# Optimization experiments

Hardware: AMD Instinct MI355X
Metric: run time of the kernel (lower is better)

Reference implementation:

```python
import jax, jax.numpy as jnp
import numpy as np

B, N, D, H, DH, DFF = 2, 2048, 1024, 16, 64, 4096
EPS = 1e-5  # F.layer_norm default


def setup_inputs() -> dict:
    key = jax.random.key(0)
    ks = jax.random.split(key, 8)
    w = lambda k, shape: jax.random.normal(k, shape, dtype=jnp.float32) * 0.02
    # standard rotary frequencies over full head dim (rot_dim = DH)
    inv_freq = 1.0 / (10000.0 ** (jnp.arange(0, DH, 2, dtype=jnp.float32) / DH))
    t = jnp.arange(N, dtype=jnp.float32)
    f = t[:, None] * inv_freq[None, :]          # [N, DH/2]
    freqs = jnp.concatenate([f, f], axis=-1)    # [N, DH]
    return {
        "x": jax.random.normal(ks[0], (B, N, D), dtype=jnp.float32),
        "gamma_pre": jnp.ones((D,), jnp.float32),
        "w_qkv": w(ks[1], (3 * D, D)),
        "w_o": w(ks[2], (D, D)),
        "gamma_ff": jnp.ones((D,), jnp.float32),
        "w_up": w(ks[3], (DFF, D)),
        "b_up": jnp.zeros((DFF,), jnp.float32),
        "w_gate": w(ks[4], (DFF, D)),
        "b_gate": jnp.zeros((DFF,), jnp.float32),
        "w_out": w(ks[5], (D, DFF)),
        "b_out": jnp.zeros((D,), jnp.float32),
        "freqs": freqs,
        "mask": jnp.ones((B, N), dtype=bool),
    }


def _layernorm(x, gamma):
    mu = jnp.mean(x, axis=-1, keepdims=True)
    var = jnp.var(x, axis=-1, keepdims=True)
    return (x - mu) * jax.lax.rsqrt(var + EPS) * gamma


def _rotate_half(x):
    x1, x2 = jnp.split(x, 2, axis=-1)
    return jnp.concatenate([-x2, x1], axis=-1)


def _rope(t, freqs):
    # rot_dim == DH so nothing is left unrotated
    return t * jnp.cos(freqs) + _rotate_half(t) * jnp.sin(freqs)


def reference(x, gamma_pre, w_qkv, w_o, gamma_ff, w_up, b_up, w_gate, b_gate,
              w_out, b_out, freqs, mask):
    b, n, d = x.shape
    # ---- self-attention branch (pre-norm) ----
    h = _layernorm(x, gamma_pre)
    qkv = h @ w_qkv.T                                   # [b, n, 3d]
    q, k, v = jnp.split(qkv, 3, axis=-1)
    to_heads = lambda t: t.reshape(b, n, H, DH).transpose(0, 2, 1, 3)  # b h n d
    q, k, v = to_heads(q), to_heads(k), to_heads(v)
    q = _rope(q, freqs)
    k = _rope(k, freqs)
    scale = 1.0 / np.sqrt(DH).astype(np.float32)
    dots = jnp.einsum('bhid,bhjd->bhij', q, k) * scale  # [b, H, n, n]
    neg = -jnp.finfo(dots.dtype).max
    dots = jnp.where(mask[:, None, None, :], dots, neg)        # key padding mask
    causal = jnp.triu(jnp.ones((n, n), dtype=bool), 1)
    dots = jnp.where(causal, neg, dots)
    attn = jax.nn.softmax(dots.astype(jnp.float32), axis=-1).astype(dots.dtype)
    o = jnp.einsum('bhij,bhjd->bhid', attn, v)
    o = o.transpose(0, 2, 1, 3).reshape(b, n, d) @ w_o.T
    o = jnp.where(mask[..., None], o, 0.0)
    x = x + o
    # ---- GLU feed-forward branch (pre-norm) ----
    h2 = _layernorm(x, gamma_ff)
    up = h2 @ w_up.T + b_up
    gate = h2 @ w_gate.T + b_gate
    ff = (up * jax.nn.silu(gate)) @ w_out.T + b_out
    return x + ff
```

## Files before the change

### kernel.cpp

```cpp
#include <hip/hip_runtime.h>
#include <stdint.h>


#define B_ 2
#define N_ 2048
#define D_ 1024
#define H_ 16
#define DFF_ 4096
#define ROWS_ (B_*N_)

typedef unsigned short u16;
typedef short short4_ __attribute__((ext_vector_type(4)));
typedef short short8 __attribute__((ext_vector_type(8)));
typedef float float4_ __attribute__((ext_vector_type(4)));

#define NEGBIG (-1e30f)
#define QSCALE 0.1803368801111204f

__device__ __forceinline__ float b2f(u16 u) {
  union { unsigned u; float f; } c; c.u = ((unsigned)u) << 16; return c.f;
}
__device__ __forceinline__ u16 f2b(float f) {
  union { float f; unsigned u; } c; c.f = f;
  unsigned x = c.u;
  x += 0x7fffu + ((x >> 16) & 1u);
  return (u16)(x >> 16);
}

__device__ __forceinline__ void gl_lds16(const u16* g, u16* l) {
  __builtin_amdgcn_global_load_lds(
      (const __attribute__((address_space(1))) unsigned int*)g,
      (__attribute__((address_space(3))) unsigned int*)l, 16, 0, 0);
}

__global__ __launch_bounds__(256) void cvt_all(const float* __restrict__ s_qkv,
                                               const float* __restrict__ s_o,
                                               const float* __restrict__ s_up,
                                               const float* __restrict__ s_gate,
                                               const float* __restrict__ s_out,
                                               u16* __restrict__ d_qkv,
                                               u16* __restrict__ d_o,
                                               u16* __restrict__ d_up,
                                               u16* __restrict__ d_gate,
                                               u16* __restrict__ d_out_) {
  int c = blockIdx.x * 256 + threadIdx.x;
  const float* src; u16* dst; int off;
  if (c < 393216)       { src = s_qkv;  dst = d_qkv;  off = c; }
  else if (c < 524288)  { src = s_o;    dst = d_o;    off = c - 393216; }
  else if (c < 1048576) { src = s_up;   dst = d_up;   off = c - 524288; }
  else if (c < 1572864) { src = s_gate; dst = d_gate; off = c - 1048576; }
  else                  { src = s_out;  dst = d_out_; off = c - 1572864; }
  int i = off * 8;
  float4_ v0 = *(const float4_*)(src + i);
  float4_ v1 = *(const float4_*)(src + i + 4);
  short8 pk;
#pragma unroll
  for (int e = 0; e < 4; e++) { pk[e] = (short)f2b(v0[e]); pk[4 + e] = (short)f2b(v1[e]); }
  *(short8*)(dst + i) = pk;
}

__global__ __launch_bounds__(256) void ln_kernel(const float* __restrict__ xin,
                                                 const float* __restrict__ gamma,
                                                 u16* __restrict__ out) {
  int row = blockIdx.x, t = threadIdx.x;
  float4_ v = *(const float4_*)(xin + (size_t)row * D_ + t * 4);
  float s = 0.f, ss = 0.f;
#pragma unroll
  for (int i = 0; i < 4; i++) { s += v[i]; ss += v[i] * v[i]; }
#pragma unroll
  for (int off = 1; off < 64; off <<= 1) {
    s  += __shfl_xor(s, off, 64);
    ss += __shfl_xor(ss, off, 64);
  }
  __shared__ float red[8];
  if ((t & 63) == 0) { red[t >> 6] = s; red[4 + (t >> 6)] = ss; }
  __syncthreads();
  s  = red[0] + red[1] + red[2] + red[3];
  ss = red[4] + red[5] + red[6] + red[7];
  float mu  = s * (1.f / D_);
  float var = ss * (1.f / D_) - mu * mu;
  float rs  = rsqrtf(var + 1e-5f);
#pragma unroll
  for (int i = 0; i < 4; i++)
    out[(size_t)row * D_ + t * 4 + i] = f2b((v[i] - mu) * rs * gamma[t * 4 + i]);
}

__global__ __launch_bounds__(256) void combine_ln(const u16* __restrict__ p0,
                                                  const u16* __restrict__ p1,
                                                  const float* __restrict__ resid,
                                                  const float* __restrict__ gamma,
                                                  float* __restrict__ x1,
                                                  u16* __restrict__ h2out) {
  int row = blockIdx.x, t = threadIdx.x;
  size_t base = (size_t)row * D_ + t * 4;
  short4_ a = *(const short4_*)(p0 + base);
  short4_ b = *(const short4_*)(p1 + base);
  float4_ rv = *(const float4_*)(resid + base);
  float4_ v;
  float s = 0.f, ss = 0.f;
#pragma unroll
  for (int i = 0; i < 4; i++) {
    v[i] = b2f((u16)a[i]) + b2f((u16)b[i]) + rv[i];
    s += v[i]; ss += v[i] * v[i];
  }
  *(float4_*)(x1 + base) = v;
#pragma unroll
  for (int off = 1; off < 64; off <<= 1) {
    s  += __shfl_xor(s, off, 64);
    ss += __shfl_xor(ss, off, 64);
  }
  __shared__ float red[8];
  if ((t & 63) == 0) { red[t >> 6] = s; red[4 + (t >> 6)] = ss; }
  __syncthreads();
  s  = red[0] + red[1] + red[2] + red[3];
  ss = red[4] + red[5] + red[6] + red[7];
  float mu  = s * (1.f / D_);
  float var = ss * (1.f / D_) - mu * mu;
  float rs  = rsqrtf(var + 1e-5f);
#pragma unroll
  for (int i = 0; i < 4; i++)
    h2out[base + i] = f2b((v[i] - mu) * rs * gamma[t * 4 + i]);
}

template <int MODE>
__device__ __forceinline__ void gemm_epilogue(float4_ (&acc)[4][4], void* Cout,
                                              const float* bias, const void* extra,
                                              int mbase, int nbase, int N,
                                              int wr, int wc, int quad, int l16) {
#pragma unroll
  for (int i = 0; i < 4; i++) {
#pragma unroll
    for (int r = 0; r < 4; r++) {
      int row = mbase + wr * 64 + i * 16 + quad * 4 + r;
#pragma unroll
      for (int j = 0; j < 4; j++) {
        int col = nbase + wc * 64 + j * 16 + l16;
        size_t idx = (size_t)row * N + col;
        float v = acc[i][j][r];
        if (MODE == 0) {
          ((u16*)Cout)[idx] = f2b(v);
        } else if (MODE == 1) {
          ((u16*)Cout)[idx] = f2b(v + bias[col]);
        } else if (MODE == 2) {
          ((float*)Cout)[idx] = v + ((const float*)extra)[idx];
        } else if (MODE == 3) {
          float gate = v + bias[col];
          float sig = 1.f / (1.f + expf(-gate));
          float upv = b2f(((const u16*)extra)[idx]);
          ((u16*)Cout)[idx] = f2b(upv * gate * sig);
        } else {
          ((float*)Cout)[idx] = v + bias[col] + ((const float*)extra)[idx];
        }
      }
    }
  }
}

__device__ __forceinline__ void gemm_core(const u16* A, const u16* W,
                                          float4_ (&acc)[4][4], u16* sA, u16* sW,
                                          int mbase, int nbase, int K,
                                          int klo, int khi,
                                          int wave, int lane, int wr, int wc,
                                          int quad, int l16) {
  for (int k0 = klo; k0 < khi; k0 += 32) {
    __syncthreads();
#pragma unroll
    for (int it = 0; it < 2; it++) {
      int c = wave * 128 + it * 64 + lane;
      int row = c >> 2, col = (c & 3) << 3;
      gl_lds16(A + (size_t)(mbase + row) * K + k0 + col, sA + (size_t)(wave * 128 + it * 64) * 8);
      gl_lds16(W + (size_t)(nbase + row) * K + k0 + col, sW + (size_t)(wave * 128 + it * 64) * 8);
    }
    __syncthreads();
    short8 af[4], bf[4];
#pragma unroll
    for (int i = 0; i < 4; i++)
      af[i] = *(const short8*)(sA + (wr * 64 + i * 16 + l16) * 32 + quad * 8);
#pragma unroll
    for (int j = 0; j < 4; j++)
      bf[j] = *(const short8*)(sW + (wc * 64 + j * 16 + l16) * 32 + quad * 8);
#pragma unroll
    for (int i = 0; i < 4; i++)
#pragma unroll
      for (int j = 0; j < 4; j++)
        acc[i][j] = __builtin_amdgcn_mfma_f32_16x16x32_bf16(af[i], bf[j], acc[i][j], 0, 0, 0);
  }
}

__global__ __launch_bounds__(256) void gemm_glu2(const u16* __restrict__ A,
                                                 const u16* __restrict__ Wu,
                                                 const u16* __restrict__ Wg,
                                                 const float* __restrict__ bu,
                                                 const float* __restrict__ bg,
                                                 u16* __restrict__ G,
                                                 int M, int N, int K) {
  __shared__ __align__(16) u16 smem[8192];
  u16* sA = smem;
  u16* sU = smem + 4096;
  u16* sG = smem + 6144;
  int t = threadIdx.x;
  int mbase = blockIdx.y * 128, nbase = blockIdx.x * 64;
  int wave = t >> 6, lane = t & 63;
  int mhalf = wave & 1, gsel = wave >> 1;
  int quad = lane >> 4, l16 = lane & 15;

  float4_ z4 = {0.f, 0.f, 0.f, 0.f};
  float4_ acc[4][4];
#pragma unroll
  for (int i = 0; i < 4; i++)
#pragma unroll
    for (int j = 0; j < 4; j++) acc[i][j] = z4;

  for (int k0 = 0; k0 < K; k0 += 32) {
    __syncthreads();
#pragma unroll
    for (int it = 0; it < 2; it++) {
      int c = it * 256 + wave * 64 + lane;
      int row = c >> 2, col = (c & 3) << 3;
      gl_lds16(A + (size_t)(mbase + row) * K + k0 + col, sA + (size_t)(it * 256 + wave * 64) * 8);
    }
    {
      int c = wave * 64 + lane;
      int row = c >> 2, col = (c & 3) << 3;
      size_t go = (size_t)(nbase + row) * K + k0 + col;
      gl_lds16(Wu + go, sU + (size_t)(wave * 64) * 8);
      gl_lds16(Wg + go, sG + (size_t)(wave * 64) * 8);
    }
    __syncthreads();
    short8 af[4], bf[4];
    const u16* sW = gsel ? sG : sU;
#pragma unroll
    for (int i = 0; i < 4; i++)
      af[i] = *(const short8*)(sA + (mhalf * 64 + i * 16 + l16) * 32 + quad * 8);
#pragma unroll
    for (int j = 0; j < 4; j++)
      bf[j] = *(const short8*)(sW + (j * 16 + l16) * 32 + quad * 8);
#pragma unroll
    for (int i = 0; i < 4; i++)
#pragma unroll
      for (int j = 0; j < 4; j++)
        acc[i][j] = __builtin_amdgcn_mfma_f32_16x16x32_bf16(af[i], bf[j], acc[i][j], 0, 0, 0);
  }

  __syncthreads();
  u16* ex = smem + mhalf * 4096;
  if (gsel) {
#pragma unroll
    for (int i = 0; i < 4; i++)
#pragma unroll
      for (int r = 0; r < 4; r++)
#pragma unroll
        for (int j = 0; j < 4; j++) {
          int col = nbase + j * 16 + l16;
          float gv = acc[i][j][r] + bg[col];
          float sig = 1.f / (1.f + expf(-gv));
          ex[(i * 16 + quad * 4 + r) * 64 + j * 16 + l16] = f2b(gv * sig);
        }
  }
  __syncthreads();
  if (!gsel) {
#pragma unroll
    for (int i = 0; i < 4; i++)
#pragma unroll
      for (int r = 0; r < 4; r++) {
        int row = mbase + mhalf * 64 + i * 16 + quad * 4 + r;
#pragma unroll
        for (int j = 0; j < 4; j++) {
          int col = nbase + j * 16 + l16;
          float uv = acc[i][j][r] + bu[col];
          float sg = b2f(ex[(i * 16 + quad * 4 + r) * 64 + j * 16 + l16]);
          G[(size_t)row * N + col] = f2b(uv * sg);
        }
      }
  }
}

__global__ __launch_bounds__(256) void gemm_bb_split(const u16* __restrict__ A,
                                                     const u16* __restrict__ W,
                                                     u16* __restrict__ p0,
                                                     u16* __restrict__ p1,
                                                     int M, int N, int K) {
  __shared__ __align__(16) u16 sA[128 * 32];
  __shared__ __align__(16) u16 sW[128 * 32];
  int t = threadIdx.x;
  int mbase = blockIdx.y * 128, nbase = blockIdx.x * 128;
  int z = blockIdx.z;
  int wave = t >> 6, lane = t & 63;
  int wr = wave >> 1, wc = wave & 1;
  int quad = lane >> 4, l16 = lane & 15;
  int Kh = K >> 1;

  float4_ z4 = {0.f, 0.f, 0.f, 0.f};
  float4_ acc[4][4];
#pragma unroll
  for (int i = 0; i < 4; i++)
#pragma unroll
    for (int j = 0; j < 4; j++) acc[i][j] = z4;

  gemm_core(A, W, acc, sA, sW, mbase, nbase, K, z * Kh, z * Kh + Kh,
            wave, lane, wr, wc, quad, l16);

  u16* P = z ? p1 : p0;
#pragma unroll
  for (int i = 0; i < 4; i++)
#pragma unroll
    for (int r = 0; r < 4; r++) {
      int row = mbase + wr * 64 + i * 16 + quad * 4 + r;
#pragma unroll
      for (int j = 0; j < 4; j++) {
        int col = nbase + wc * 64 + j * 16 + l16;
        P[(size_t)row * N + col] = f2b(acc[i][j][r]);
      }
    }
}

__global__ __launch_bounds__(256) void split_combine(const u16* __restrict__ p0,
                                                     const u16* __restrict__ p1,
                                                     const float* __restrict__ bias,
                                                     const float* __restrict__ resid,
                                                     float* __restrict__ out, int N) {
  int idx = (blockIdx.x * 256 + threadIdx.x) * 8;
  int col = idx & (N - 1);
  short8 a = *(const short8*)(p0 + idx);
  short8 b = *(const short8*)(p1 + idx);
  float4_ r0 = *(const float4_*)(resid + idx);
  float4_ r1 = *(const float4_*)(resid + idx + 4);
  float4_ o0, o1;
#pragma unroll
  for (int e = 0; e < 4; e++) {
    float bb0 = bias ? bias[col + e] : 0.f;
    float bb1 = bias ? bias[col + 4 + e] : 0.f;
    o0[e] = b2f((u16)a[e]) + b2f((u16)b[e]) + bb0 + r0[e];
    o1[e] = b2f((u16)a[4 + e]) + b2f((u16)b[4 + e]) + bb1 + r1[e];
  }
  *(float4_*)(out + idx) = o0;
  *(float4_*)(out + idx + 4) = o1;
}

template <int MODE>
__global__ __launch_bounds__(256) void gemm_nt(const u16* __restrict__ A,
                                               const float* __restrict__ W,
                                               void* Cout,
                                               const float* __restrict__ bias,
                                               const void* extra,
                                               int M, int N, int K) {
  __shared__ __align__(16) u16 sA[128 * 32];
  __shared__ __align__(16) u16 sW[128 * 32];
  int t = threadIdx.x;
  int mbase = blockIdx.y * 128, nbase = blockIdx.x * 128;
  int wave = t >> 6, lane = t & 63;
  int wr = wave >> 1, wc = wave & 1;
  int quad = lane >> 4, l16 = lane & 15;

  float4_ z4 = {0.f, 0.f, 0.f, 0.f};
  float4_ acc[4][4];
#pragma unroll
  for (int i = 0; i < 4; i++)
#pragma unroll
    for (int j = 0; j < 4; j++) acc[i][j] = z4;

  for (int k0 = 0; k0 < K; k0 += 32) {
    __syncthreads();
#pragma unroll
    for (int it = 0; it < 2; it++) {
      int c = t + 256 * it;
      int row = c >> 2, col = (c & 3) << 3;
      ((short8*)sA)[c] = *(const short8*)(A + (size_t)(mbase + row) * K + k0 + col);
      const float* wp = W + (size_t)(nbase + row) * K + k0 + col;
      float4_ w0 = *(const float4_*)wp;
      float4_ w1 = *(const float4_*)(wp + 4);
      short8 pk;
#pragma unroll
      for (int e = 0; e < 4; e++) { pk[e] = (short)f2b(w0[e]); pk[4 + e] = (short)f2b(w1[e]); }
      ((short8*)sW)[c] = pk;
    }
    __syncthreads();
    short8 af[4], bf[4];
#pragma unroll
    for (int i = 0; i < 4; i++)
      af[i] = *(const short8*)(sA + (wr * 64 + i * 16 + l16) * 32 + quad * 8);
#pragma unroll
    for (int j = 0; j < 4; j++)
      bf[j] = *(const short8*)(sW + (wc * 64 + j * 16 + l16) * 32 + quad * 8);
#pragma unroll
    for (int i = 0; i < 4; i++)
#pragma unroll
      for (int j = 0; j < 4; j++)
        acc[i][j] = __builtin_amdgcn_mfma_f32_16x16x32_bf16(af[i], bf[j], acc[i][j], 0, 0, 0);
  }
  gemm_epilogue<MODE>(acc, Cout, bias, extra, mbase, nbase, N, wr, wc, quad, l16);
}

template <int SPLIT>
__global__ __launch_bounds__(256) void rope_kernel(const u16* __restrict__ q0,
                                                   const u16* __restrict__ q1,
                                                   const float* __restrict__ freqs,
                                                   u16* __restrict__ qr,
                                                   u16* __restrict__ kr,
                                                   u16* __restrict__ vt) {
  int idx = blockIdx.x * 256 + threadIdx.x;
  int d2 = idx & 31;
  int h  = (idx >> 5) & 15;
  int n  = (idx >> 9) & 2047;
  int b  = idx >> 20;
  float f = freqs[n * 64 + d2];
  float c = cosf(f), s = sinf(f);
  size_t base = (size_t)(b * N_ + n) * 3072;
  int hd = h * 64 + d2;
#define LD(o) (SPLIT ? (b2f(q0[base + (o)]) + b2f(q1[base + (o)])) : b2f(q0[base + (o)]))
  float v_q1 = LD(hd),        v_q2 = LD(hd + 32);
  float v_k1 = LD(1024 + hd), v_k2 = LD(1024 + hd + 32);
  float v_v1 = LD(2048 + hd), v_v2 = LD(2048 + hd + 32);
#undef LD
  size_t ro = ((size_t)(b * H_ + h) * N_ + n) * 64 + d2;
  qr[ro]      = f2b((v_q1 * c - v_q2 * s) * QSCALE);
  qr[ro + 32] = f2b((v_q2 * c + v_q1 * s) * QSCALE);
  kr[ro]      = f2b(v_k1 * c - v_k2 * s);
  kr[ro + 32] = f2b(v_k2 * c + v_k1 * s);
  size_t vo = ((size_t)(b * H_ + h) * 64 + d2) * N_ + n;
  vt[vo]           = f2b(v_v1);
  vt[vo + 32 * N_] = f2b(v_v2);
}

#define LP 72
__global__ __launch_bounds__(256) void attn_kernel(const u16* __restrict__ qr,
                                                   const u16* __restrict__ kr,
                                                   const u16* __restrict__ vt,
                                                   u16* __restrict__ opart,
                                                   float* __restrict__ mlp) {
  __shared__ __align__(16) u16 sK[64 * LP];
  __shared__ __align__(16) u16 sV[64 * LP];
  __shared__ __align__(16) u16 sP[4][16 * LP];
  int qp = blockIdx.x, bh = blockIdx.y, sp = blockIdx.z;
  int t = threadIdx.x, wave = t >> 6, lane = t & 63;
  int quad = lane >> 4, l16 = lane & 15;
  const u16* qptr = qr + (size_t)bh * N_ * 64;
  const u16* kp = kr + (size_t)bh * N_ * 64;
  const u16* vp = vt + (size_t)bh * 64 * N_;
  float4_ z4 = {0.f, 0.f, 0.f, 0.f};

  for (int qsel = 0; qsel < 2; qsel++) {
    int qt = qsel ? (N_ / 64 - 1 - qp) : qp;
    int qbase = qt * 64;
    int ntiles = qt + 1, half = (ntiles + 1) >> 1;
    int ktlo = sp ? half : 0, kthi = sp ? ntiles : half;

    short8 aq[2];
    int qrow = qbase + wave * 16 + l16;
#pragma unroll
    for (int kk = 0; kk < 2; kk++)
      aq[kk] = *(const short8*)(qptr + (size_t)qrow * 64 + kk * 32 + quad * 8);

    float4_ o[4] = {z4, z4, z4, z4};
    float m_r[4] = {NEGBIG, NEGBIG, NEGBIG, NEGBIG};
    float l_r[4] = {0.f, 0.f, 0.f, 0.f};

    for (int kt = ktlo; kt < kthi; kt++) {
      __syncthreads();
      {
        const u16* src = kp + (size_t)kt * 64 * 64;
#pragma unroll
        for (int it = 0; it < 2; it++) {
          int c = t + 256 * it;
          int row = c >> 3, seg = c & 7;
          *(short8*)(sK + row * LP + seg * 8) = *(const short8*)(src + c * 8);
          *(short8*)(sV + row * LP + seg * 8) =
              *(const short8*)(vp + (size_t)row * N_ + kt * 64 + seg * 8);
        }
      }
      __syncthreads();

      float4_ sf[4];
#pragma unroll
      for (int j = 0; j < 4; j++) {
        short8 bk0 = *(const short8*)(sK + (j * 16 + l16) * LP + quad * 8);
        short8 bk1 = *(const short8*)(sK + (j * 16 + l16) * LP + 32 + quad * 8);
        float4_ acc = z4;
        acc = __builtin_amdgcn_mfma_f32_16x16x32_bf16(aq[0], bk0, acc, 0, 0, 0);
        acc = __builtin_amdgcn_mfma_f32_16x16x32_bf16(aq[1], bk1, acc, 0, 0, 0);
        sf[j] = acc;
      }
      if (kt == qt) {
#pragma unroll
        for (int j = 0; j < 4; j++)
#pragma unroll
          for (int r = 0; r < 4; r++) {
            int ig = qbase + wave * 16 + quad * 4 + r;
            int jg = kt * 64 + j * 16 + l16;
            if (jg > ig) sf[j][r] = NEGBIG;
          }
      }

#pragma unroll
      for (int r = 0; r < 4; r++) {
        float mt = fmaxf(fmaxf(sf[0][r], sf[1][r]), fmaxf(sf[2][r], sf[3][r]));
#pragma unroll
        for (int off = 1; off < 16; off <<= 1) mt = fmaxf(mt, __shfl_xor(mt, off, 64));
        float mn = fmaxf(m_r[r], mt);
        float alpha = exp2f(m_r[r] - mn);
        float rowsum = 0.f;
#pragma unroll
        for (int j = 0; j < 4; j++) {
          float p = exp2f(sf[j][r] - mn);
          sf[j][r] = p;
          rowsum += p;
        }
#pragma unroll
        for (int off = 1; off < 16; off <<= 1) rowsum += __shfl_xor(rowsum, off, 64);
        l_r[r] = l_r[r] * alpha + rowsum;
        m_r[r] = mn;
#pragma unroll
        for (int jo = 0; jo < 4; jo++) o[jo][r] *= alpha;
      }

      u16* sPw = sP[wave];
#pragma unroll
      for (int j = 0; j < 4; j++)
#pragma unroll
        for (int r = 0; r < 4; r++)
          sPw[(quad * 4 + r) * LP + j * 16 + l16] = f2b(sf[j][r]);
      short8 ap[2];
#pragma unroll
      for (int kk = 0; kk < 2; kk++)
        ap[kk] = *(const short8*)(sPw + l16 * LP + kk * 32 + quad * 8);
#pragma unroll
      for (int jo = 0; jo < 4; jo++)
#pragma unroll
        for (int kk = 0; kk < 2; kk++) {
          short8 bv = *(const short8*)(sV + (jo * 16 + l16) * LP + kk * 32 + quad * 8);
          o[jo] = __builtin_amdgcn_mfma_f32_16x16x32_bf16(ap[kk], bv, o[jo], 0, 0, 0);
        }
    }

#pragma unroll
    for (int r = 0; r < 4; r++) {
      int n = qbase + wave * 16 + quad * 4 + r;
      size_t row = (size_t)bh * N_ + n;
      if (l16 == 0) {
        mlp[2 * (sp * (size_t)65536 + row)]     = m_r[r];
        mlp[2 * (sp * (size_t)65536 + row) + 1] = l_r[r];
      }
#pragma unroll
      for (int jo = 0; jo < 4; jo++)
        opart[sp * (size_t)4194304 + row * 64 + jo * 16 + l16] = f2b(o[jo][r]);
    }
  }
}

__global__ __launch_bounds__(256) void attn_combine(const u16* __restrict__ opart,
                                                    const float* __restrict__ mlp,
                                                    u16* __restrict__ obuf) {
  int idx = blockIdx.x * 256 + threadIdx.x;
  int row = idx >> 3, seg = idx & 7;
  float m0 = mlp[2 * row],                 l0 = mlp[2 * row + 1];
  float m1 = mlp[2 * (65536 + row)],       l1 = mlp[2 * (65536 + row) + 1];
  float mmax = fmaxf(m0, m1);
  float w0 = exp2f(m0 - mmax), w1 = exp2f(m1 - mmax);
  float inv = 1.f / (l0 * w0 + l1 * w1);
  short8 a = *(const short8*)(opart + (size_t)row * 64 + seg * 8);
  short8 b = *(const short8*)(opart + (size_t)4194304 + (size_t)row * 64 + seg * 8);
  short8 r;
#pragma unroll
  for (int e = 0; e < 8; e++)
    r[e] = (short)f2b((b2f((u16)a[e]) * w0 + b2f((u16)b[e]) * w1) * inv);
  int bh = row >> 11, n = row & 2047;
  int bb = bh >> 4, h = bh & 15;
  *(short8*)(obuf + ((size_t)(bb * N_ + n) * D_) + h * 64 + seg * 8) = r;
}

extern "C" void kernel_launch(void* const* d_in, const int* in_sizes, int n_in,
                              void* d_out, int out_size, void* d_ws, size_t ws_size,
                              hipStream_t stream) {
  const float* x         = (const float*)d_in[0];
  const float* gamma_pre = (const float*)d_in[1];
  const float* w_qkv     = (const float*)d_in[2];
  const float* w_o       = (const float*)d_in[3];
  const float* gamma_ff  = (const float*)d_in[4];
  const float* w_up      = (const float*)d_in[5];
  const float* b_up      = (const float*)d_in[6];
  const float* w_gate    = (const float*)d_in[7];
  const float* b_gate    = (const float*)d_in[8];
  const float* w_out     = (const float*)d_in[9];
  const float* b_out     = (const float*)d_in[10];
  const float* freqs     = (const float*)d_in[11];

  char* ws = (char*)d_ws;
  const size_t MB = 1024 * 1024;
  float* out = (float*)d_out;
  bool wide = ws_size >= 96 * MB;

  if (wide) {
    u16*  h     = (u16*)(ws);
    u16*  qp0   = (u16*)(ws + 32 * MB);
    u16*  qp1   = (u16*)(ws + 8 * MB);
    u16*  qr    = (u16*)(ws + 56 * MB);
    u16*  kr    = (u16*)d_out;
    u16*  vtb   = (u16*)d_out + 4194304;
    u16*  opart = (u16*)(ws);
    float* mlb  = (float*)(ws + 16 * MB);
    u16*  ob    = (u16*)(ws + 24 * MB);
    u16*  sp0   = (u16*)(ws);
    u16*  sp1o  = (u16*)(ws + 32 * MB);
    float* x1   = (float*)(ws + 8 * MB);
    u16*  h2    = (u16*)(ws + 24 * MB);
    u16*  g     = (u16*)(ws + 32 * MB);
    u16*  sp1f  = (u16*)(ws + 24 * MB);
    u16* wb_qkv  = (u16*)(ws + 64 * MB);
    u16* wb_o    = (u16*)(ws + 70 * MB);
    u16* wb_up   = (u16*)(ws + 72 * MB);
    u16* wb_gate = (u16*)(ws + 80 * MB);
    u16* wb_out  = (u16*)(ws + 88 * MB);

    cvt_all<<<8192, 256, 0, stream>>>(w_qkv, w_o, w_up, w_gate, w_out,
                                      wb_qkv, wb_o, wb_up, wb_gate, wb_out);
    ln_kernel<<<ROWS_, 256, 0, stream>>>(x, gamma_pre, h);
    gemm_bb_split<<<dim3(3072 / 128, ROWS_ / 128, 2), 256, 0, stream>>>(
        h, wb_qkv, qp0, qp1, ROWS_, 3072, 1024);
    rope_kernel<1><<<(B_ * N_ * H_ * 32) / 256, 256, 0, stream>>>(
        qp0, qp1, freqs, qr, kr, vtb);
    attn_kernel<<<dim3(N_ / 128, B_ * H_, 2), 256, 0, stream>>>(qr, kr, vtb, opart, mlb);
    attn_combine<<<(B_ * H_ * N_ * 8) / 256, 256, 0, stream>>>(opart, mlb, ob);
    gemm_bb_split<<<dim3(1024 / 128, ROWS_ / 128, 2), 256, 0, stream>>>(
        ob, wb_o, sp0, sp1o, ROWS_, 1024, 1024);
    combine_ln<<<ROWS_, 256, 0, stream>>>(sp0, sp1o, x, gamma_ff, x1, h2);
    gemm_glu2<<<dim3(4096 / 64, ROWS_ / 128), 256, 0, stream>>>(
        h2, wb_up, wb_gate, b_up, b_gate, g, ROWS_, 4096, 1024);
    gemm_bb_split<<<dim3(1024 / 128, ROWS_ / 128, 2), 256, 0, stream>>>(
        g, wb_out, sp0, sp1f, ROWS_, 1024, 4096);
    split_combine<<<(ROWS_ * 1024) / 2048, 256, 0, stream>>>(
        sp0, sp1f, b_out, x1, out, 1024);
  } else {
    u16*  h     = (u16*)(ws);
    u16*  qkv   = (u16*)(ws + 8 * MB);
    u16*  qr    = (u16*)(ws + 32 * MB);
    u16*  kr    = (u16*)(ws + 40 * MB);
    u16*  vtb   = (u16*)(ws + 48 * MB);
    u16*  ob    = (u16*)(ws + 56 * MB);
    u16*  opart = (u16*)(ws);
    float* mlb  = (float*)(ws + 16 * MB);
    float* x1   = (float*)(ws + 8 * MB);
    u16*  h2    = (u16*)(ws + 24 * MB);
    u16*  g     = (u16*)(ws + 32 * MB);

    ln_kernel<<<ROWS_, 256, 0, stream>>>(x, gamma_pre, h);
    gemm_nt<0><<<dim3(3072 / 128, ROWS_ / 128), 256, 0, stream>>>(
        h, w_qkv, qkv, nullptr, nullptr, ROWS_, 3072, 1024);
    rope_kernel<0><<<(B_ * N_ * H_ * 32) / 256, 256, 0, stream>>>(
        qkv, qkv, freqs, qr, kr, vtb);
    attn_kernel<<<dim3(N_ / 128, B_ * H_, 2), 256, 0, stream>>>(qr, kr, vtb, opart, mlb);
    attn_combine<<<(B_ * H_ * N_ * 8) / 256, 256, 0, stream>>>(opart, mlb, ob);
    gemm_nt<2><<<dim3(1024 / 128, ROWS_ / 128), 256, 0, stream>>>(
        ob, w_o, x1, nullptr, x, ROWS_, 1024, 1024);
    ln_kernel<<<ROWS_, 256, 0, stream>>>(x1, gamma_ff, h2);
    gemm_nt<1><<<dim3(4096 / 128, ROWS_ / 128), 256, 0, stream>>>(
        h2, w_up, g, b_up, nullptr, ROWS_, 4096, 1024);
    gemm_nt<3><<<dim3(4096 / 128, ROWS_ / 128), 256, 0, stream>>>(
        h2, w_gate, g, b_gate, g, ROWS_, 4096, 1024);
    gemm_nt<4><<<dim3(1024 / 128, ROWS_ / 128), 256, 0, stream>>>(
        g, w_out, (void*)out, b_out, x1, ROWS_, 1024, 4096);
  }
}
```

Measured before the change: 505.8 us.

## Split attention KV range four ways and deepen GLU GEMM K-step to 64

Result: faster. 485.6 us (-4.0%).

```diff
diff --git a/kernel.cpp b/kernel.cpp
--- a/kernel.cpp
+++ b/kernel.cpp
@@ -85,12 +85,12 @@
     out[(size_t)row * D_ + t * 4 + i] = f2b((v[i] - mu) * rs * gamma[t * 4 + i]);
 }
 
-__global__ __launch_bounds__(256) void combine_ln(const u16* __restrict__ p0,
+__global__ __launch_bounds__(256) void combine_ln(const u16* p0,
                                                   const u16* __restrict__ p1,
                                                   const float* __restrict__ resid,
                                                   const float* __restrict__ gamma,
                                                   float* __restrict__ x1,
-                                                  u16* __restrict__ h2out) {
+                                                  u16* h2out) {
   int row = blockIdx.x, t = threadIdx.x;
   size_t base = (size_t)row * D_ + t * 4;
   short4_ a = *(const short4_*)(p0 + base);
@@ -194,10 +194,10 @@
                                                  const float* __restrict__ bg,
                                                  u16* __restrict__ G,
                                                  int M, int N, int K) {
-  __shared__ __align__(16) u16 smem[8192];
+  __shared__ __align__(16) u16 smem[16384];
   u16* sA = smem;
-  u16* sU = smem + 4096;
-  u16* sG = smem + 6144;
+  u16* sU = smem + 8192;
+  u16* sG = smem + 12288;
   int t = threadIdx.x;
   int mbase = blockIdx.y * 128, nbase = blockIdx.x * 64;
   int wave = t >> 6, lane = t & 63;
@@ -211,35 +211,42 @@
 #pragma unroll
     for (int j = 0; j < 4; j++) acc[i][j] = z4;
 
-  for (int k0 = 0; k0 < K; k0 += 32) {
+  for (int k0 = 0; k0 < K; k0 += 64) {
     __syncthreads();
 #pragma unroll
-    for (int it = 0; it < 2; it++) {
-      int c = it * 256 + wave * 64 + lane;
-      int row = c >> 2, col = (c & 3) << 3;
-      gl_lds16(A + (size_t)(mbase + row) * K + k0 + col, sA + (size_t)(it * 256 + wave * 64) * 8);
-    }
-    {
+    for (int hh = 0; hh < 2; hh++) {
+      int kh = k0 + hh * 32;
+#pragma unroll
+      for (int it = 0; it < 2; it++) {
+        int c = it * 256 + wave * 64 + lane;
+        int row = c >> 2, col = (c & 3) << 3;
+        gl_lds16(A + (size_t)(mbase + row) * K + kh + col,
+                 sA + hh * 4096 + (size_t)(it * 256 + wave * 64) * 8);
+      }
       int c = wave * 64 + lane;
       int row = c >> 2, col = (c & 3) << 3;
-      size_t go = (size_t)(nbase + row) * K + k0 + col;
-      gl_lds16(Wu + go, sU + (size_t)(wave * 64) * 8);
-      gl_lds16(Wg + go, sG + (size_t)(wave * 64) * 8);
+      size_t go = (size_t)(nbase + row) * K + kh + col;
+      gl_lds16(Wu + go, sU + hh * 2048 + (size_t)(wave * 64) * 8);
+      gl_lds16(Wg + go, sG + hh * 2048 + (size_t)(wave * 64) * 8);
     }
     __syncthreads();
-    short8 af[4], bf[4];
-    const u16* sW = gsel ? sG : sU;
-#pragma unroll
-    for (int i = 0; i < 4; i++)
-      af[i] = *(const short8*)(sA + (mhalf * 64 + i * 16 + l16) * 32 + quad * 8);
-#pragma unroll
-    for (int j = 0; j < 4; j++)
-      bf[j] = *(const short8*)(sW + (j * 16 + l16) * 32 + quad * 8);
-#pragma unroll
-    for (int i = 0; i < 4; i++)
+#pragma unroll
+    for (int hh = 0; hh < 2; hh++) {
+      short8 af[4], bf[4];
+      const u16* sAp = sA + hh * 4096;
+      const u16* sWp = (gsel ? sG : sU) + hh * 2048;
+#pragma unroll
+      for (int i = 0; i < 4; i++)
+        af[i] = *(const short8*)(sAp + (mhalf * 64 + i * 16 + l16) * 32 + quad * 8);
 #pragma unroll
       for (int j = 0; j < 4; j++)
-        acc[i][j] = __builtin_amdgcn_mfma_f32_16x16x32_bf16(af[i], bf[j], acc[i][j], 0, 0, 0);
+        bf[j] = *(const short8*)(sWp + (j * 16 + l16) * 32 + quad * 8);
+#pragma unroll
+      for (int i = 0; i < 4; i++)
+#pragma unroll
+        for (int j = 0; j < 4; j++)
+          acc[i][j] = __builtin_amdgcn_mfma_f32_16x16x32_bf16(af[i], bf[j], acc[i][j], 0, 0, 0);
+    }
   }
 
   __syncthreads();
@@ -423,6 +430,7 @@
 }
 
 #define LP 72
+#define NSPLIT 4
 __global__ __launch_bounds__(256) void attn_kernel(const u16* __restrict__ qr,
                                                    const u16* __restrict__ kr,
                                                    const u16* __restrict__ vt,
@@ -442,8 +450,8 @@
   for (int qsel = 0; qsel < 2; qsel++) {
     int qt = qsel ? (N_ / 64 - 1 - qp) : qp;
     int qbase = qt * 64;
-    int ntiles = qt + 1, half = (ntiles + 1) >> 1;
-    int ktlo = sp ? half : 0, kthi = sp ? ntiles : half;
+    int ntiles = qt + 1;
+    int ktlo = (ntiles * sp) / NSPLIT, kthi = (ntiles * (sp + 1)) / NSPLIT;
 
     short8 aq[2];
     int qrow = qbase + wave * 16 + l16;
@@ -552,17 +560,28 @@
                                                     u16* __restrict__ obuf) {
   int idx = blockIdx.x * 256 + threadIdx.x;
   int row = idx >> 3, seg = idx & 7;
-  float m0 = mlp[2 * row],                 l0 = mlp[2 * row + 1];
-  float m1 = mlp[2 * (65536 + row)],       l1 = mlp[2 * (65536 + row) + 1];
-  float mmax = fmaxf(m0, m1);
-  float w0 = exp2f(m0 - mmax), w1 = exp2f(m1 - mmax);
-  float inv = 1.f / (l0 * w0 + l1 * w1);
-  short8 a = *(const short8*)(opart + (size_t)row * 64 + seg * 8);
-  short8 b = *(const short8*)(opart + (size_t)4194304 + (size_t)row * 64 + seg * 8);
+  float mm[NSPLIT], ll[NSPLIT];
+  float mmax = NEGBIG;
+#pragma unroll
+  for (int s = 0; s < NSPLIT; s++) {
+    mm[s] = mlp[2 * (s * (size_t)65536 + row)];
+    ll[s] = mlp[2 * (s * (size_t)65536 + row) + 1];
+    mmax = fmaxf(mmax, mm[s]);
+  }
+  float w[NSPLIT], lsum = 0.f;
+#pragma unroll
+  for (int s = 0; s < NSPLIT; s++) { w[s] = exp2f(mm[s] - mmax); lsum += ll[s] * w[s]; }
+  float inv = 1.f / lsum;
+  float acc[8] = {0, 0, 0, 0, 0, 0, 0, 0};
+#pragma unroll
+  for (int s = 0; s < NSPLIT; s++) {
+    short8 a = *(const short8*)(opart + s * (size_t)4194304 + (size_t)row * 64 + seg * 8);
+#pragma unroll
+    for (int e = 0; e < 8; e++) acc[e] += b2f((u16)a[e]) * w[s];
+  }
   short8 r;
 #pragma unroll
-  for (int e = 0; e < 8; e++)
-    r[e] = (short)f2b((b2f((u16)a[e]) * w0 + b2f((u16)b[e]) * w1) * inv);
+  for (int e = 0; e < 8; e++) r[e] = (short)f2b(acc[e] * inv);
   int bh = row >> 11, n = row & 2047;
   int bb = bh >> 4, h = bh & 15;
   *(short8*)(obuf + ((size_t)(bb * N_ + n) * D_) + h * 64 + seg * 8) = r;
@@ -591,20 +610,21 @@
 
   if (wide) {
     u16*  h     = (u16*)(ws);
-    u16*  qp0   = (u16*)(ws + 32 * MB);
-    u16*  qp1   = (u16*)(ws + 8 * MB);
+    u16*  qp0   = (u16*)(ws + 8 * MB);
+    u16*  qp1   = (u16*)(ws + 32 * MB);
     u16*  qr    = (u16*)(ws + 56 * MB);
     u16*  kr    = (u16*)d_out;
     u16*  vtb   = (u16*)d_out + 4194304;
     u16*  opart = (u16*)(ws);
-    float* mlb  = (float*)(ws + 16 * MB);
-    u16*  ob    = (u16*)(ws + 24 * MB);
+    float* mlb  = (float*)(ws + 32 * MB);
+    u16*  ob    = (u16*)(ws + 34 * MB);
     u16*  sp0   = (u16*)(ws);
-    u16*  sp1o  = (u16*)(ws + 32 * MB);
-    float* x1   = (float*)(ws + 8 * MB);
-    u16*  h2    = (u16*)(ws + 24 * MB);
+    u16*  sp1o  = (u16*)(ws + 8 * MB);
+    float* x1   = (float*)(ws + 16 * MB);
+    u16*  h2    = (u16*)(ws);
     u16*  g     = (u16*)(ws + 32 * MB);
-    u16*  sp1f  = (u16*)(ws + 24 * MB);
+    u16*  sp0f  = (u16*)(ws);
+    u16*  sp1f  = (u16*)(ws + 8 * MB);
     u16* wb_qkv  = (u16*)(ws + 64 * MB);
     u16* wb_o    = (u16*)(ws + 70 * MB);
     u16* wb_up   = (u16*)(ws + 72 * MB);
@@ -618,7 +638,8 @@
         h, wb_qkv, qp0, qp1, ROWS_, 3072, 1024);
     rope_kernel<1><<<(B_ * N_ * H_ * 32) / 256, 256, 0, stream>>>(
         qp0, qp1, freqs, qr, kr, vtb);
-    attn_kernel<<<dim3(N_ / 128, B_ * H_, 2), 256, 0, stream>>>(qr, kr, vtb, opart, mlb);
+    attn_kernel<<<dim3(N_ / 128, B_ * H_, NSPLIT), 256, 0, stream>>>(
+        qr, kr, vtb, opart, mlb);
     attn_combine<<<(B_ * H_ * N_ * 8) / 256, 256, 0, stream>>>(opart, mlb, ob);
     gemm_bb_split<<<dim3(1024 / 128, ROWS_ / 128, 2), 256, 0, stream>>>(
         ob, wb_o, sp0, sp1o, ROWS_, 1024, 1024);
@@ -626,9 +647,9 @@
     gemm_glu2<<<dim3(4096 / 64, ROWS_ / 128), 256, 0, stream>>>(
         h2, wb_up, wb_gate, b_up, b_gate, g, ROWS_, 4096, 1024);
     gemm_bb_split<<<dim3(1024 / 128, ROWS_ / 128, 2), 256, 0, stream>>>(
-        g, wb_out, sp0, sp1f, ROWS_, 1024, 4096);
+        g, wb_out, sp0f, sp1f, ROWS_, 1024, 4096);
     split_combine<<<(ROWS_ * 1024) / 2048, 256, 0, stream>>>(
-        sp0, sp1f, b_out, x1, out, 1024);
+        sp0f, sp1f, b_out, x1, out, 1024);
   } else {
     u16*  h     = (u16*)(ws);
     u16*  qkv   = (u16*)(ws + 8 * MB);
@@ -637,7 +658,7 @@
     u16*  vtb   = (u16*)(ws + 48 * MB);
     u16*  ob    = (u16*)(ws + 56 * MB);
     u16*  opart = (u16*)(ws);
-    float* mlb  = (float*)(ws + 16 * MB);
+    float* mlb  = (float*)(ws + 32 * MB);
     float* x1   = (float*)(ws + 8 * MB);
     u16*  h2    = (u16*)(ws + 24 * MB);
     u16*  g     = (u16*)(ws + 32 * MB);
@@ -647,8 +668,10 @@
         h, w_qkv, qkv, nullptr, nullptr, ROWS_, 3072, 1024);
     rope_kernel<0><<<(B_ * N_ * H_ * 32) / 256, 256, 0, stream>>>(
         qkv, qkv, freqs, qr, kr, vtb);
-    attn_kernel<<<dim3(N_ / 128, B_ * H_, 2), 256, 0, stream>>>(qr, kr, vtb, opart, mlb);
-    attn_combine<<<(B_ * H_ * N_ * 8) / 256, 256, 0, stream>>>(opart, mlb, ob);
+    attn_kernel<<<dim3(N_ / 128, B_ * H_, NSPLIT), 256, 0, stream>>>(
+        qr, kr, vtb, (u16*)(ws), (float*)(ws + 32 * MB));
+    attn_combine<<<(B_ * H_ * N_ * 8) / 256, 256, 0, stream>>>(
+        (u16*)(ws), (float*)(ws + 32 * MB), ob);
     gemm_nt<2><<<dim3(1024 / 128, ROWS_ / 128), 256, 0, stream>>>(
         ob, w_o, x1, nullptr, x, ROWS_, 1024, 1024);
     ln_kernel<<<ROWS_, 256, 0, stream>>>(x1, gamma_ff, h2);
```
